# Kernel optimization log

Hardware: AMD Instinct MI355X
Metric: run time of the kernel (lower is better)

The kernel has to match this reference:

```python
import jax, jax.numpy as jnp
import numpy as np

N = 131072
E = 524288
H = 128
EPS = 1e-5

def _layernorm(h, g, b):
    mu = jnp.mean(h, axis=-1, keepdims=True)
    var = jnp.mean((h - mu) ** 2, axis=-1, keepdims=True)
    return (h - mu) * jax.lax.rsqrt(var + EPS) * g + b

def _node_to_node(x, senders, receivers, valid, num_nodes, params):
    # two-way (symmetrized) message passing: gather + scatter_add, then MLP+LN
    W1, b1, W2, b2, W3, b3, g, beta = params
    tws = jnp.concatenate([senders, receivers])
    twr = jnp.concatenate([receivers, senders])
    msg = x[tws]  # [2E', H] gather
    if valid is not None:
        msg = jnp.where(jnp.concatenate([valid, valid])[:, None], msg, 0.0)
    agg = jax.ops.segment_sum(msg, twr, num_segments=num_nodes)  # scatter_add
    h = jax.nn.gelu(agg @ W1 + b1, approximate=False)
    h = jax.nn.gelu(h @ W2 + b2, approximate=False)
    h = h @ W3 + b3
    return _layernorm(h, g, beta)

def setup_inputs() -> dict:
    key = jax.random.key(0)
    ks = jax.random.split(key, 20)
    s = 0.05
    inp = {
        "x": jax.random.normal(ks[0], (N, H), dtype=jnp.float32),
        "edge_index": jax.random.randint(ks[1], (2, E), 0, N, dtype=jnp.int32),
        "pool_p": jax.random.normal(ks[2], (H,), dtype=jnp.float32),
    }
    names = ["dW1", "db1", "dW2", "db2", "dW3", "db3", "dg", "dbeta",
             "uW1", "ub1", "uW2", "ub2", "uW3", "ub3", "ug", "ubeta"]
    shapes = [(H, H), (H,), (H, H), (H,), (H, H), (H,), (H,), (H,),
              (2 * H, H), (H,), (H, H), (H,), (H, H), (H,), (H,), (H,)]
    for i, (nm, sh) in enumerate(zip(names, shapes)):
        if nm in ("dg", "ug"):
            inp[nm] = jnp.ones(sh, dtype=jnp.float32)
        elif nm in ("dbeta", "ubeta") or nm.startswith(("db", "ub")):
            inp[nm] = jnp.zeros(sh, dtype=jnp.float32)
        else:
            inp[nm] = jax.random.normal(ks[3 + i], sh, dtype=jnp.float32) * s
    return inp

def reference(x, edge_index, pool_p,
              dW1, db1, dW2, db2, dW3, db3, dg, dbeta,
              uW1, ub1, uW2, ub2, uW3, ub3, ug, ubeta):
    senders, receivers = edge_index[0], edge_index[1]
    k = N // 2  # TopKPooling ratio=0.5

    # ---- down: TopKPooling ----
    score = x @ pool_p / jnp.linalg.norm(pool_p)  # [N]
    _, perm = jax.lax.top_k(score, k)             # kept node indices
    x_skip = x
    x_p = x[perm] * jnp.tanh(score[perm])[:, None]  # [k, H]
    mask = jnp.zeros((N,), dtype=bool).at[perm].set(True)
    mapping = jnp.zeros((N,), dtype=jnp.int32).at[perm].set(
        jnp.arange(k, dtype=jnp.int32))
    valid = mask[senders] & mask[receivers]
    ps, pr = mapping[senders], mapping[receivers]

    # down conv on pooled graph
    x_d = _node_to_node(x_p, ps, pr, valid, k,
                        (dW1, db1, dW2, db2, dW3, db3, dg, dbeta))

    # ---- up: unpool (indexed scatter write) + skip concat + up conv ----
    recovered = jnp.zeros_like(x_skip).at[perm].set(x_d)
    x_u = jnp.concatenate([recovered, x_skip], axis=-1)  # [N, 2H]
    out = _node_to_node(x_u, senders, receivers, None, N,
                        (uW1, ub1, uW2, ub2, uW3, ub3, ug, ubeta))
    return out
```

## Files before the change

kernel.cpp:

```cpp
#include <hip/hip_runtime.h>

#define N_NODES 131072
#define N_EDGES 524288
#define K_TOP   65536
#define LN_EPS  1e-5f
#define N_TILES (N_NODES / 64)
#define K_TILES (K_TOP / 64)
#define BCAP    5120u

typedef unsigned int u32;
typedef unsigned short u16;
typedef unsigned long long u64;

typedef __attribute__((ext_vector_type(8))) short bf8;
typedef __attribute__((ext_vector_type(4))) float f4;

#define ST_OFF    0
#define CANON_OFF (64u<<10)
#define PART_OFF  (576u<<10)
#define KEYS_OFF  (1u<<20)
#define TVAL_OFF  (2u<<20)
#define KEPT_OFF  ((2u<<20)+(512u<<10))
#define SBUF_OFF  (3u<<20)
#define ADJ_OFF   (35u<<20)


#define C_DW1 0
#define C_DB1 16384
#define C_DW2 16512
#define C_DB2 32896
#define C_DW3 33024
#define C_DB3 49408
#define C_DG  49536
#define C_DBE 49664
#define C_UW1 49792
#define C_UB1 82560
#define C_UW2 82688
#define C_UB2 99072
#define C_UW3 99200
#define C_UB3 115584
#define C_UG  115712
#define C_UBE 115840
#define C_TOT 115968
#define CT_DW1 115968
#define CT_DW2 132352
#define CT_DW3 148736
#define CT_UW1 165120
#define CT_UW2 197888
#define CT_UW3 214272
#define CT_TOT 230656

__device__ __forceinline__ float bflo(u32 u){ return __uint_as_float(u << 16); }
__device__ __forceinline__ float bfhi(u32 u){ return __uint_as_float(u & 0xFFFF0000u); }
__device__ __forceinline__ float bf2f(u16 v){ return __uint_as_float(((u32)v) << 16); }
__device__ __forceinline__ u32 f2bf(float f){
  u32 u = __float_as_uint(f);
  return (u + 0x7FFFu + ((u >> 16) & 1u)) >> 16;
}
__device__ __forceinline__ float gelu_f(float x){
  return 0.5f * x * (1.0f + erff(x * 0.7071067811865476f));
}
__device__ __forceinline__ float2 f2add(float2 a, float2 b){
  return make_float2(a.x + b.x, a.y + b.y);
}

__device__ __forceinline__ int swz16(int row, int cc){
  return row * 128 + ((cc ^ (row & 15)) * 8);
}

__device__ __forceinline__ bf8 ld_bf16_chunk(const u32* __restrict__ rowp, int s, int quad){
  uint4 v = *(const uint4*)(rowp + s * 16 + quad * 4);
  return __builtin_bit_cast(bf8, v);
}
__device__ __forceinline__ bf8 scale_bf16_chunk(const u32* __restrict__ rowp, int s, int quad, float tv){
  uint4 v = *(const uint4*)(rowp + s * 16 + quad * 4);
  uint4 q;
  q.x = f2bf(bflo(v.x) * tv) | (f2bf(bfhi(v.x) * tv) << 16);
  q.y = f2bf(bflo(v.y) * tv) | (f2bf(bfhi(v.y) * tv) << 16);
  q.z = f2bf(bflo(v.z) * tv) | (f2bf(bfhi(v.z) * tv) << 16);
  q.w = f2bf(bflo(v.w) * tv) | (f2bf(bfhi(v.w) * tv) << 16);
  return __builtin_bit_cast(bf8, q);
}
__device__ __forceinline__ bf8 cvt_f32_chunk(const float* __restrict__ rowp, int s, int quad, float tv){
  const float* p = rowp + s * 32 + quad * 8;
  float4 f0 = *(const float4*)p;
  float4 f1 = *(const float4*)(p + 4);
  uint4 q;
  q.x = f2bf(f0.x * tv) | (f2bf(f0.y * tv) << 16);
  q.y = f2bf(f0.z * tv) | (f2bf(f0.w * tv) << 16);
  q.z = f2bf(f1.x * tv) | (f2bf(f1.y * tv) << 16);
  q.w = f2bf(f1.z * tv) | (f2bf(f1.w * tv) << 16);
  return __builtin_bit_cast(bf8, q);
}

__device__ __forceinline__ void gemm_ab(const u16* ws, const bf8 a[4], int mn, int quad, f4 acc[8]){
  #pragma unroll
  for (int s = 0; s < 4; s++){
    #pragma unroll
    for (int j = 0; j < 8; j++){
      bf8 b = *(const bf8*)&ws[swz16(j * 16 + mn, s * 4 + quad)];
      acc[j] = __builtin_amdgcn_mfma_f32_16x16x32_bf16(a[s], b, acc[j], 0, 0, 0);
    }
  }
}

struct SelState {
  u64 prefix;
  u32 krem, eqcnt;
  int is_f32;
  u32 pad;
  double inv_norm;
  u32 eqlist[4096];
  u64 eqkey[4096];
};

struct P16 { const void* q[16]; };

__device__ __forceinline__ void chain_step(const u32* __restrict__ tots, int q,
                                           u32* sfx, u32* selb, int t,
                                           u64& pref, u32& target){
  sfx[t] = tots[q * 256 + t];
  __syncthreads();
  for (int o = 1; o < 256; o <<= 1){
    u32 x = (t + o < 256) ? sfx[t + o] : 0u;
    __syncthreads();
    sfx[t] += x;
    __syncthreads();
  }
  u32 above = (t == 255) ? 0u : sfx[t + 1];
  if (sfx[t] >= target && above < target){ selb[0] = (u32)t; selb[1] = target - above; }
  __syncthreads();
  pref = (pref << 8) | (u64)selb[0];
  target = selb[1];
  __syncthreads();
}

__global__ void k_detect(const u32* __restrict__ xw, SelState* st){
  int t = threadIdx.x;
  int cnt = 0;
  for (int i = t; i < 4096; i += 256){
    u32 w = xw[(size_t)i * 2048];
    u32 e = (w >> 23) & 0xFFu;
    if (e >= 97u && e <= 135u) cnt++;
  }
  __shared__ int sh[256];
  sh[t] = cnt; __syncthreads();
  for (int o = 128; o > 0; o >>= 1){ if (t < o) sh[t] += sh[t+o]; __syncthreads(); }
  if (t == 0){
    st->is_f32 = (sh[0] >= 3072) ? 1 : 0;
    st->prefix = 0; st->krem = K_TOP; st->eqcnt = 0;
  }
}

__global__ void k_canon(P16 ps, const SelState* __restrict__ st, u16* __restrict__ canon,
                        u32* __restrict__ tots, u32* __restrict__ gcur){
  int i = blockIdx.x * 256 + threadIdx.x;
  if (i < 1024) tots[i] = 0u;
  if (i < 256)  gcur[i] = (u32)i * BCAP;
  if (i >= CT_TOT) return;
  int isf = st->is_f32;
  if (i < C_TOT){
    const int off[17] = {C_DW1,C_DB1,C_DW2,C_DB2,C_DW3,C_DB3,C_DG,C_DBE,
                         C_UW1,C_UB1,C_UW2,C_UB2,C_UW3,C_UB3,C_UG,C_UBE,C_TOT};
    int seg = 0;
    #pragma unroll
    for (int s2 = 0; s2 < 16; s2++) if (i >= off[s2+1]) seg = s2 + 1;
    int j = i - off[seg];
    if (isf) canon[i] = (u16)f2bf(((const float*)ps.q[seg])[j]);
    else     canon[i] = ((const u16*)ps.q[seg])[j];
  } else {
    const int dst[7] = {CT_DW1, CT_DW2, CT_DW3, CT_UW1, CT_UW2, CT_UW3, CT_TOT};
    const int wq[6]  = {0, 2, 4, 8, 10, 12};
    int g = i;
    int seg = 0;
    #pragma unroll
    for (int s2 = 0; s2 < 6; s2++) if (g >= dst[s2+1]) seg = s2 + 1;
    int loc = g - dst[seg];
    int K = (seg == 3) ? 256 : 128;
    int n = loc / K, k = loc % K;
    int src = k * 128 + n;
    if (isf) canon[g] = (u16)f2bf(((const float*)ps.q[wq[seg]])[src]);
    else     canon[g] = ((const u16*)ps.q[wq[seg]])[src];
  }
}

__global__ __launch_bounds__(256) void k_score(const void* __restrict__ xraw, const void* __restrict__ praw,
                        const SelState* __restrict__ st,
                        u64* __restrict__ keys, float* __restrict__ tval){
  int t = threadIdx.x, lane = t & 63, w = t >> 6;
  int n = blockIdx.x * 4 + w;
  double d, ps;
  if (st->is_f32){
    const float* xf = (const float*)xraw + (size_t)n * 128;
    const float* pf = (const float*)praw;
    double p0 = (double)pf[lane], p1 = (double)pf[64 + lane];
    d  = (double)xf[lane] * p0 + (double)xf[64 + lane] * p1;
    ps = p0 * p0 + p1 * p1;
  } else {
    const u32* xw = (const u32*)xraw + (size_t)n * 64;
    const u32* pw = (const u32*)praw;
    u32 xx = xw[lane], pv = pw[lane];
    double p0 = (double)bflo(pv), p1 = (double)bfhi(pv);
    d  = (double)bflo(xx) * p0 + (double)bfhi(xx) * p1;
    ps = p0 * p0 + p1 * p1;
  }
  for (int o = 32; o > 0; o >>= 1){
    d  += __shfl_down(d,  o, 64);
    ps += __shfl_down(ps, o, 64);
  }
  if (lane == 0){
    double sc = d * (1.0 / sqrt(ps));
    u64 u = (u64)__double_as_longlong(sc);
    u64 key = (u & 0x8000000000000000ULL) ? ~u : (u | 0x8000000000000000ULL);
    keys[n] = key;
    tval[n] = tanhf((float)sc);
  }
}

__global__ __launch_bounds__(256) void k_histp(const u64* __restrict__ keys,
                                               u32* __restrict__ tots, int pass){
  __shared__ u32 sfx[256];
  __shared__ u32 selb[2];
  __shared__ u32 h[256];
  int t = threadIdx.x;
  u64 pref = 0;
  u32 target = K_TOP;
  for (int q = 0; q < pass; q++)
    chain_step(tots, q, sfx, selb, t, pref, target);
  h[t] = 0;
  __syncthreads();
  int sh_d = 56 - 8 * pass;
  for (int n = blockIdx.x * 256 + t; n < N_NODES; n += 256 * 256){
    u64 k = keys[n];
    bool m = (pass == 0) ? true : ((k >> (sh_d + 8)) == pref);
    if (m) atomicAdd(&h[(u32)((k >> sh_d) & 255)], 1u);
  }
  __syncthreads();
  if (h[t]) atomicAdd(&tots[pass * 256 + t], h[t]);
}

__global__ __launch_bounds__(256) void k_mark(const u64* __restrict__ keys,
                                              const u32* __restrict__ tots,
                                              SelState* st, u32* __restrict__ kept){
  __shared__ u32 sfx[256];
  __shared__ u32 selb[2];
  int t = threadIdx.x;
  u64 pref = 0;
  u32 target = K_TOP;
  for (int q = 0; q < 4; q++)
    chain_step(tots, q, sfx, selb, t, pref, target);
  u32 T = (u32)pref;
  int n = blockIdx.x * 256 + t;
  u64 k = keys[n];
  u32 t32 = (u32)(k >> 32);
  kept[n] = (t32 > T) ? 1u : 0u;
  if (t32 == T){
    u32 i = atomicAdd(&st->eqcnt, 1u);
    if (i < 4096){ st->eqlist[i] = (u32)n; st->eqkey[i] = k; }
  }
}

__global__ __launch_bounds__(256) void k_tie(const u32* __restrict__ tots,
                                             SelState* st, u32* __restrict__ kept){
  __shared__ u32 sfx[256];
  __shared__ u32 selb[2];
  int t = threadIdx.x;
  u64 pref = 0;
  u32 target = K_TOP;
  for (int q = 0; q < 4; q++)
    chain_step(tots, q, sfx, selb, t, pref, target);
  u32 r = target;
  u32 m = st->eqcnt; if (m > 4096) m = 4096;
  for (u32 i = t; i < m; i += 256){
    u64 ki = st->eqkey[i]; u32 ii = st->eqlist[i];
    u32 rank = 0;
    for (u32 j = 0; j < m; j++){
      u64 kj = st->eqkey[j];
      rank += (kj > ki || (kj == ki && st->eqlist[j] < ii)) ? 1u : 0u;
    }
    if (rank < r) kept[ii] = 1u;
  }
}

__global__ __launch_bounds__(256) void k_psum(const u32* __restrict__ kept, u32* __restrict__ bsum){
  __shared__ u32 sh[256];
  int t = threadIdx.x;
  sh[t] = kept[blockIdx.x * 256 + t];
  __syncthreads();
  for (int o = 128; o > 0; o >>= 1){ if (t < o) sh[t] += sh[t+o]; __syncthreads(); }
  if (t == 0) bsum[blockIdx.x] = sh[0];
}

__global__ void k_pscan(u32* __restrict__ bsum){
  __shared__ u32 ex2[256];
  int t = threadIdx.x;
  u32 c0 = bsum[2 * t], c1 = bsum[2 * t + 1];
  ex2[t] = c0 + c1;
  __syncthreads();
  for (int o = 1; o < 256; o <<= 1){
    u32 x = (t >= o) ? ex2[t - o] : 0u;
    __syncthreads();
    ex2[t] += x;
    __syncthreads();
  }
  u32 e0 = ex2[t] - c0 - c1;
  bsum[2 * t] = e0;
  bsum[2 * t + 1] = e0 + c0;
}

__global__ __launch_bounds__(256) void k_pwrite(const u32* __restrict__ kept,
                                                const u32* __restrict__ bsum,
                                                u32* __restrict__ perm){
  __shared__ u32 sc[256];
  int t = threadIdx.x;
  int n = blockIdx.x * 256 + t;
  u32 kp = kept[n];
  sc[t] = kp;
  __syncthreads();
  for (int o = 1; o < 256; o <<= 1){
    u32 x = (t >= o) ? sc[t - o] : 0u;
    __syncthreads();
    sc[t] += x;
    __syncthreads();
  }
  if (kp) perm[bsum[blockIdx.x] + sc[t] - 1u] = (u32)n;
}

__global__ __launch_bounds__(256) void k_bin(const int* __restrict__ se, const int* __restrict__ re,
                                             u32* __restrict__ gcur, u32* __restrict__ pairs){
  __shared__ u32 cnt[256], sc[256], base[256], cur[256], gpos[256];
  __shared__ u32 stage[8192];
  int t = threadIdx.x;
  cnt[t] = 0;
  __syncthreads();
  int e0 = blockIdx.x * 4096;
  for (int i = t; i < 4096; i += 256){
    int s = se[e0 + i], r = re[e0 + i];
    atomicAdd(&cnt[(u32)r >> 9], 1u);
    atomicAdd(&cnt[(u32)s >> 9], 1u);
  }
  __syncthreads();
  sc[t] = cnt[t];
  __syncthreads();
  for (int o = 1; o < 256; o <<= 1){
    u32 x = (t >= o) ? sc[t - o] : 0u;
    __syncthreads();
    sc[t] += x;
    __syncthreads();
  }
  base[t] = sc[t] - cnt[t];
  cur[t] = base[t];
  gpos[t] = atomicAdd(&gcur[t], cnt[t]);
  __syncthreads();
  for (int i = t; i < 4096; i += 256){
    u32 s = (u32)se[e0 + i], r = (u32)re[e0 + i];
    u32 b1 = r >> 9, p1 = ((r & 511u) << 17) | s;
    u32 b2 = s >> 9, p2 = ((s & 511u) << 17) | r;
    stage[atomicAdd(&cur[b1], 1u)] = p1;
    stage[atomicAdd(&cur[b2], 1u)] = p2;
  }
  __syncthreads();
  int lane = t & 63, wv = t >> 6;
  for (int b = wv; b < 256; b += 4){
    u32 n = cnt[b], src = base[b], dst = gpos[b];
    for (u32 i = lane; i < n; i += 64)
      pairs[dst + i] = stage[src + i];
  }
}

__global__ __launch_bounds__(256) void k_place(const u32* __restrict__ gcur,
                                               const u32* __restrict__ pairs,
                                               const u32* __restrict__ kept,
                                               u32* __restrict__ adj,
                                               u32* __restrict__ off, u32* __restrict__ cnts){
  __shared__ u32 cnt[512], ck[512], curk[512], curn[512], lo[512], ex2[256];
  int b = blockIdx.x, t = threadIdx.x;
  u32 base = (u32)b * BCAP;
  u32 total = gcur[b] - base;
  cnt[t] = 0; cnt[t + 256] = 0;
  ck[t] = 0;  ck[t + 256] = 0;
  curk[t] = 0; curk[t + 256] = 0;
  curn[t] = 0; curn[t + 256] = 0;
  __syncthreads();
  for (u32 i = t; i < total; i += 256){
    u32 p = pairs[base + i];
    u32 nl = p >> 17, m = p & 0x1FFFFu;
    atomicAdd(&cnt[nl], 1u);
    if (kept[m]) atomicAdd(&ck[nl], 1u);
  }
  __syncthreads();
  u32 c0 = cnt[2 * t], c1 = cnt[2 * t + 1];
  ex2[t] = c0 + c1;
  __syncthreads();
  for (int o = 1; o < 256; o <<= 1){
    u32 x = (t >= o) ? ex2[t - o] : 0u;
    __syncthreads();
    ex2[t] += x;
    __syncthreads();
  }
  u32 e0 = ex2[t] - c0 - c1;
  int n0 = b * 512 + 2 * t;
  off[n0]     = base + e0;
  off[n0 + 1] = base + e0 + c0;
  cnts[n0]     = (ck[2 * t] << 16) | c0;
  cnts[n0 + 1] = (ck[2 * t + 1] << 16) | c1;
  lo[2 * t] = e0; lo[2 * t + 1] = e0 + c0;
  __syncthreads();
  for (u32 i = t; i < total; i += 256){
    u32 p = pairs[base + i];
    u32 nl = p >> 17, m = p & 0x1FFFFu;
    u32 slot;
    if (kept[m]) slot = base + lo[nl] + atomicAdd(&curk[nl], 1u);
    else         slot = base + lo[nl] + ck[nl] + atomicAdd(&curn[nl], 1u);
    adj[slot] = m;
  }
}


__global__ __launch_bounds__(256, 3) void k_proj_down(
    const void* __restrict__ xraw, const float* __restrict__ tval,
    const u16* __restrict__ W1T, const SelState* __restrict__ st,
    const u32* __restrict__ kept, u32* __restrict__ S)
{
  __shared__ u16 w1s[128 * 128];
  __shared__ u16 os[64 * 128];
  int t = threadIdx.x, lane = t & 63, wv = t >> 6;
  int m0 = wv * 16, mn = lane & 15, quad = lane >> 4;

  for (int i = t; i < 2048; i += 256){
    int row = i >> 4, cc = i & 15;
    *(uint4*)&w1s[swz16(row, cc)] = *(const uint4*)(W1T + row * 128 + cc * 8);
  }
  int isf = st->is_f32;
  __syncthreads();

  for (int tile = blockIdx.x; tile < N_TILES; tile += gridDim.x){
    int row0 = tile * 64;
    int arow = row0 + m0 + mn;
    float tv = tval[arow];
    bf8 a[4];
    if (isf){
      const float* xf = (const float*)xraw + (size_t)arow * 128;
      #pragma unroll
      for (int s = 0; s < 4; s++) a[s] = cvt_f32_chunk(xf, s, quad, tv);
    } else {
      const u32* xw = (const u32*)xraw + (size_t)arow * 64;
      #pragma unroll
      for (int s = 0; s < 4; s++) a[s] = scale_bf16_chunk(xw, s, quad, tv);
    }
    f4 acc[8];
    #pragma unroll
    for (int j = 0; j < 8; j++){ acc[j][0]=0.f; acc[j][1]=0.f; acc[j][2]=0.f; acc[j][3]=0.f; }
    gemm_ab(w1s, a, mn, quad, acc);

    #pragma unroll
    for (int j = 0; j < 8; j++){
      int c = j * 16 + mn;
      #pragma unroll
      for (int rg = 0; rg < 4; rg++){
        int row = m0 + quad * 4 + rg;
        os[row * 128 + ((c >> 3) ^ (row & 15)) * 8 + (c & 7)] = (u16)f2bf(acc[j][rg]);
      }
    }
    __builtin_amdgcn_wave_barrier();
    int rl = m0 + (lane >> 2), qt = lane & 3;
    u32 kp = kept[row0 + rl];
    u32* out = S + (size_t)(row0 + rl) * 64;
    if (kp){
      #pragma unroll
      for (int i = 0; i < 4; i++){
        int cc = qt * 4 + i;
        *(uint4*)(out + cc * 4) = *(const uint4*)&os[swz16(rl, cc)];
      }
    }
    __builtin_amdgcn_wave_barrier();
  }
}

__global__ __launch_bounds__(256, 2) void k_proj_up(
    const u32* __restrict__ R, const void* __restrict__ xraw,
    const u16* __restrict__ W1T, const SelState* __restrict__ st,
    const u32* __restrict__ kept, u32* __restrict__ S2)
{
  __shared__ u16 was[128 * 128];
  __shared__ u16 wbs[128 * 128];
  __shared__ u16 os[64 * 128];
  int t = threadIdx.x, lane = t & 63, wv = t >> 6;
  int m0 = wv * 16, mn = lane & 15, quad = lane >> 4;

  for (int i = t; i < 2048; i += 256){
    int row = i >> 4, cc = i & 15;
    *(uint4*)&was[swz16(row, cc)] = *(const uint4*)(W1T + row * 256 + cc * 8);
    *(uint4*)&wbs[swz16(row, cc)] = *(const uint4*)(W1T + row * 256 + 128 + cc * 8);
  }
  int isf = st->is_f32;
  __syncthreads();

  for (int tile = blockIdx.x; tile < N_TILES; tile += gridDim.x){
    int row0 = tile * 64;
    int arow = row0 + m0 + mn;
    bf8 a[4];
    u32 kp = kept[arow];
    const u32* rp = R + (size_t)arow * 64;
    #pragma unroll
    for (int s = 0; s < 4; s++){
      if (kp) a[s] = ld_bf16_chunk(rp, s, quad);
      else { uint4 z = {0,0,0,0}; a[s] = __builtin_bit_cast(bf8, z); }
    }
    f4 acc[8];
    #pragma unroll
    for (int j = 0; j < 8; j++){ acc[j][0]=0.f; acc[j][1]=0.f; acc[j][2]=0.f; acc[j][3]=0.f; }
    gemm_ab(was, a, mn, quad, acc);

    if (isf){
      const float* xf = (const float*)xraw + (size_t)arow * 128;
      #pragma unroll
      for (int s = 0; s < 4; s++) a[s] = cvt_f32_chunk(xf, s, quad, 1.0f);
    } else {
      const u32* xw = (const u32*)xraw + (size_t)arow * 64;
      #pragma unroll
      for (int s = 0; s < 4; s++) a[s] = ld_bf16_chunk(xw, s, quad);
    }
    gemm_ab(wbs, a, mn, quad, acc);

    #pragma unroll
    for (int j = 0; j < 8; j++){
      int c = j * 16 + mn;
      #pragma unroll
      for (int rg = 0; rg < 4; rg++){
        int row = m0 + quad * 4 + rg;
        os[row * 128 + ((c >> 3) ^ (row & 15)) * 8 + (c & 7)] = (u16)f2bf(acc[j][rg]);
      }
    }
    __builtin_amdgcn_wave_barrier();
    int rl = m0 + (lane >> 2), qt = lane & 3;
    u32* out = S2 + (size_t)(row0 + rl) * 64;
    #pragma unroll
    for (int i = 0; i < 4; i++){
      int cc = qt * 4 + i;
      *(uint4*)(out + cc * 4) = *(const uint4*)&os[swz16(rl, cc)];
    }
    __builtin_amdgcn_wave_barrier();
  }
}

__device__ __forceinline__ void agg_row(const u32* __restrict__ Smsg, const u32* __restrict__ adj,
                                        u32 jb, u32 je, int lane, float b1l, float b1h,
                                        u32* __restrict__ Hrow){
  float2 a = make_float2(0.f, 0.f);
  u32 j = jb;
  for (; j + 8 <= je; j += 8){
    u32 e0 = adj[j],   e1 = adj[j+1], e2 = adj[j+2], e3 = adj[j+3];
    u32 e4 = adj[j+4], e5 = adj[j+5], e6 = adj[j+6], e7 = adj[j+7];
    u32 w0 = Smsg[(size_t)e0 * 64 + lane];
    u32 w1 = Smsg[(size_t)e1 * 64 + lane];
    u32 w2 = Smsg[(size_t)e2 * 64 + lane];
    u32 w3 = Smsg[(size_t)e3 * 64 + lane];
    u32 w4 = Smsg[(size_t)e4 * 64 + lane];
    u32 w5 = Smsg[(size_t)e5 * 64 + lane];
    u32 w6 = Smsg[(size_t)e6 * 64 + lane];
    u32 w7 = Smsg[(size_t)e7 * 64 + lane];
    float2 v0 = make_float2(bflo(w0), bfhi(w0));
    float2 v1 = make_float2(bflo(w1), bfhi(w1));
    float2 v2 = make_float2(bflo(w2), bfhi(w2));
    float2 v3 = make_float2(bflo(w3), bfhi(w3));
    float2 v4 = make_float2(bflo(w4), bfhi(w4));
    float2 v5 = make_float2(bflo(w5), bfhi(w5));
    float2 v6 = make_float2(bflo(w6), bfhi(w6));
    float2 v7 = make_float2(bflo(w7), bfhi(w7));
    a = f2add(a, f2add(f2add(f2add(v0, v1), f2add(v2, v3)),
                       f2add(f2add(v4, v5), f2add(v6, v7))));
  }
  for (; j + 4 <= je; j += 4){
    u32 e0 = adj[j], e1 = adj[j+1], e2 = adj[j+2], e3 = adj[j+3];
    u32 w0 = Smsg[(size_t)e0 * 64 + lane];
    u32 w1 = Smsg[(size_t)e1 * 64 + lane];
    u32 w2 = Smsg[(size_t)e2 * 64 + lane];
    u32 w3 = Smsg[(size_t)e3 * 64 + lane];
    float2 v0 = make_float2(bflo(w0), bfhi(w0));
    float2 v1 = make_float2(bflo(w1), bfhi(w1));
    float2 v2 = make_float2(bflo(w2), bfhi(w2));
    float2 v3 = make_float2(bflo(w3), bfhi(w3));
    a = f2add(a, f2add(f2add(v0, v1), f2add(v2, v3)));
  }
  for (; j < je; j++){
    u32 w = Smsg[(size_t)adj[j] * 64 + lane];
    a = f2add(a, make_float2(bflo(w), bfhi(w)));
  }
  Hrow[lane] = f2bf(gelu_f(a.x + b1l)) | (f2bf(gelu_f(a.y + b1h)) << 16);
}

__global__ __launch_bounds__(256, 4) void k_agg_up(
    const u32* __restrict__ Smsg, const u32* __restrict__ off, const u32* __restrict__ cnts,
    const u32* __restrict__ adj, const u16* __restrict__ cb1,
    u32* __restrict__ H)
{
  int t = threadIdx.x, lane = t & 63, wv = t >> 6;
  float b1l = bf2f(cb1[2 * lane]), b1h = bf2f(cb1[2 * lane + 1]);
  int base = blockIdx.x * 16 + wv * 4;
  #pragma unroll 1
  for (int rr = 0; rr < 4; rr++){
    int n = base + rr;
    u32 jb = off[n];
    agg_row(Smsg, adj, jb, jb + (cnts[n] & 0xFFFFu), lane, b1l, b1h, H + (size_t)n * 64);
  }
}

__global__ __launch_bounds__(256, 4) void k_agg_down(
    const u32* __restrict__ Smsg, const u32* __restrict__ off, const u32* __restrict__ cnts,
    const u32* __restrict__ adj, const u16* __restrict__ cb1,
    const u32* __restrict__ perm, u32* __restrict__ H)
{
  int t = threadIdx.x, lane = t & 63, wv = t >> 6;
  float b1l = bf2f(cb1[2 * lane]), b1h = bf2f(cb1[2 * lane + 1]);
  int base = blockIdx.x * 16 + wv * 4;
  #pragma unroll 1
  for (int rr = 0; rr < 4; rr++){
    int n = (int)perm[base + rr];
    u32 jb = off[n];
    agg_row(Smsg, adj, jb, jb + (cnts[n] >> 16), lane, b1l, b1h, H + (size_t)n * 64);
  }
}

template<int IS_DOWN>
__global__ __launch_bounds__(256, 2) void k_mlp(
    const u32* __restrict__ H,
    const u16* __restrict__ cW2T, const u16* __restrict__ cb2,
    const u16* __restrict__ cW3T, const u16* __restrict__ cb3,
    const u16* __restrict__ cg, const u16* __restrict__ cbe,
    const u32* __restrict__ perm, const SelState* __restrict__ st,
    u32* __restrict__ Rout, void* __restrict__ fout)
{
  __shared__ u16 w2s[128 * 128];
  __shared__ u16 w3s[128 * 128];
  __shared__ u16 os[64 * 128];
  int t = threadIdx.x, lane = t & 63, wv = t >> 6;
  int m0 = wv * 16, mn = lane & 15, quad = lane >> 4;

  for (int i = t; i < 2048; i += 256){
    int row = i >> 4, cc = i & 15;
    *(uint4*)&w2s[swz16(row, cc)] = *(const uint4*)(cW2T + row * 128 + cc * 8);
    *(uint4*)&w3s[swz16(row, cc)] = *(const uint4*)(cW3T + row * 128 + cc * 8);
  }
  float b2v[8], b3v[8], gv[8], bev[8];
  #pragma unroll
  for (int j = 0; j < 8; j++){
    int c = j * 16 + mn;
    b2v[j] = bf2f(cb2[c]); b3v[j] = bf2f(cb3[c]);
    gv[j]  = bf2f(cg[c]);  bev[j] = bf2f(cbe[c]);
  }
  int isf = st->is_f32;
  int ntiles = IS_DOWN ? K_TILES : N_TILES;
  __syncthreads();

  for (int tile = blockIdx.x; tile < ntiles; tile += gridDim.x){
    int row0 = tile * 64;
    int arow = IS_DOWN ? (int)perm[row0 + m0 + mn] : (row0 + m0 + mn);

    bf8 a[4];
    const u32* hp = H + (size_t)arow * 64;
    #pragma unroll
    for (int s = 0; s < 4; s++) a[s] = ld_bf16_chunk(hp, s, quad);
    f4 acc[8];
    #pragma unroll
    for (int j = 0; j < 8; j++){ acc[j][0]=0.f; acc[j][1]=0.f; acc[j][2]=0.f; acc[j][3]=0.f; }
    gemm_ab(w2s, a, mn, quad, acc);

    #pragma unroll
    for (int j = 0; j < 8; j++){
      int c = j * 16 + mn;
      #pragma unroll
      for (int rg = 0; rg < 4; rg++){
        int row = m0 + quad * 4 + rg;
        os[row * 128 + ((c >> 3) ^ (row & 15)) * 8 + (c & 7)] = (u16)f2bf(gelu_f(acc[j][rg] + b2v[j]));
      }
    }
    __builtin_amdgcn_wave_barrier();

    #pragma unroll
    for (int s = 0; s < 4; s++) a[s] = *(const bf8*)&os[swz16(m0 + mn, s * 4 + quad)];
    #pragma unroll
    for (int j = 0; j < 8; j++){ acc[j][0]=0.f; acc[j][1]=0.f; acc[j][2]=0.f; acc[j][3]=0.f; }
    gemm_ab(w3s, a, mn, quad, acc);

    #pragma unroll
    for (int j = 0; j < 8; j++){
      #pragma unroll
      for (int rg = 0; rg < 4; rg++) acc[j][rg] += b3v[j];
    }
    float s1[4] = {0.f,0.f,0.f,0.f}, s2[4] = {0.f,0.f,0.f,0.f};
    #pragma unroll
    for (int j = 0; j < 8; j++){
      #pragma unroll
      for (int rg = 0; rg < 4; rg++){
        float v = acc[j][rg];
        s1[rg] += v; s2[rg] += v * v;
      }
    }
    #pragma unroll
    for (int o = 1; o < 16; o <<= 1){
      #pragma unroll
      for (int rg = 0; rg < 4; rg++){
        s1[rg] += __shfl_xor(s1[rg], o, 64);
        s2[rg] += __shfl_xor(s2[rg], o, 64);
      }
    }
    float mu[4], rs[4];
    #pragma unroll
    for (int rg = 0; rg < 4; rg++){
      mu[rg] = s1[rg] * 0.0078125f;
      float var = s2[rg] * 0.0078125f - mu[rg] * mu[rg];
      rs[rg] = rsqrtf(var + LN_EPS);
    }
    #pragma unroll
    for (int j = 0; j < 8; j++){
      #pragma unroll
      for (int rg = 0; rg < 4; rg++)
        acc[j][rg] = (acc[j][rg] - mu[rg]) * rs[rg] * gv[j] + bev[j];
    }

    if (!IS_DOWN && isf){
      float* fo = (float*)fout;
      #pragma unroll
      for (int j = 0; j < 8; j++){
        #pragma unroll
        for (int rg = 0; rg < 4; rg++)
          fo[(size_t)(row0 + m0 + quad * 4 + rg) * 128 + j * 16 + mn] = acc[j][rg];
      }
      continue;
    }

    __builtin_amdgcn_wave_barrier();
    #pragma unroll
    for (int j = 0; j < 8; j++){
      int c = j * 16 + mn;
      #pragma unroll
      for (int rg = 0; rg < 4; rg++){
        int row = m0 + quad * 4 + rg;
        os[row * 128 + ((c >> 3) ^ (row & 15)) * 8 + (c & 7)] = (u16)f2bf(acc[j][rg]);
      }
    }
    __builtin_amdgcn_wave_barrier();
    int rl = m0 + (lane >> 2), qt = lane & 3;
    int orow = IS_DOWN ? (int)perm[row0 + rl] : (row0 + rl);
    u32* out = (IS_DOWN ? Rout : (u32*)fout) + (size_t)orow * 64;
    #pragma unroll
    for (int i = 0; i < 4; i++){
      int cc = qt * 4 + i;
      *(uint4*)(out + cc * 4) = *(const uint4*)&os[swz16(rl, cc)];
    }
    __builtin_amdgcn_wave_barrier();
  }
}


extern "C" void kernel_launch(void* const* d_in, const int* in_sizes, int n_in,
                              void* d_out, int out_size, void* d_ws, size_t ws_size,
                              hipStream_t stream)
{
  const void* x     = d_in[0];
  const int* eidx   = (const int*)d_in[1];
  const void* poolp = d_in[2];
  const int* senders = eidx;
  const int* receivers = eidx + N_EDGES;

  char* ws = (char*)d_ws;
  SelState* st = (SelState*)(ws + ST_OFF);
  u16*  canon  = (u16*) (ws + CANON_OFF);
  u32*  tots   = (u32*) (ws + PART_OFF);
  u32*  gcur   = (u32*) (ws + PART_OFF + 4096);
  u32*  bsum   = (u32*) (ws + PART_OFF + 8192);
  u32*  perm   = (u32*) (ws + PART_OFF + 16384);
  u64*  keys   = (u64*) (ws + KEYS_OFF);
  u32*  off    = (u32*) (ws + KEYS_OFF);
  u32*  cnts   = (u32*) (ws + KEYS_OFF + (512u<<10));
  float* tval  = (float*)(ws + TVAL_OFF);
  u32*  kept   = (u32*) (ws + KEPT_OFF);
  u32*  Sbuf   = (u32*) (ws + SBUF_OFF);
  u32*  adj    = (u32*) (ws + ADJ_OFF);
  u32*  pairs  = Sbuf;
  u32*  Dbuf   = (u32*) d_out;

  P16 ps;
  for (int i = 0; i < 16; i++) ps.q[i] = d_in[3 + i];

  k_detect<<<1, 256, 0, stream>>>((const u32*)x, st);
  k_canon<<<(CT_TOT + 255) / 256, 256, 0, stream>>>(ps, st, canon, tots, gcur);
  k_score<<<N_NODES / 4, 256, 0, stream>>>(x, poolp, st, keys, tval);
  for (int pass = 0; pass < 4; pass++)
    k_histp<<<256, 256, 0, stream>>>(keys, tots, pass);
  k_mark<<<N_NODES / 256, 256, 0, stream>>>(keys, tots, st, kept);
  k_tie<<<1, 256, 0, stream>>>(tots, st, kept);

  k_psum<<<N_NODES / 256, 256, 0, stream>>>(kept, bsum);
  k_pscan<<<1, 256, 0, stream>>>(bsum);
  k_pwrite<<<N_NODES / 256, 256, 0, stream>>>(kept, bsum, perm);

  k_bin<<<N_EDGES / 4096, 256, 0, stream>>>(senders, receivers, gcur, pairs);
  k_place<<<256, 256, 0, stream>>>(gcur, pairs, kept, adj, off, cnts);

  k_proj_down<<<768, 256, 0, stream>>>(x, tval, canon + CT_DW1, st, kept, Sbuf);
  k_agg_down<<<K_TOP / 16, 256, 0, stream>>>(Sbuf, off, cnts, adj, canon + C_DB1, perm, Dbuf);
  k_mlp<1><<<512, 256, 0, stream>>>(Dbuf,
      canon + CT_DW2, canon + C_DB2, canon + CT_DW3, canon + C_DB3,
      canon + C_DG, canon + C_DBE, perm, st, Sbuf, nullptr);

  k_proj_up<<<512, 256, 0, stream>>>(Sbuf, x, canon + CT_UW1, st, kept, Dbuf);
  k_agg_up<<<N_NODES / 16, 256, 0, stream>>>(Dbuf, off, cnts, adj, canon + C_UB1, Sbuf);
  k_mlp<0><<<512, 256, 0, stream>>>(Sbuf,
      canon + CT_UW2, canon + C_UB2, canon + CT_UW3, canon + C_UB3,
      canon + C_UG, canon + C_UBE, perm, st, nullptr, d_out);
}
```

Measured before the change: 442.0 us.

## Store pooled features compactly by rank and prefetch next MLP tile

k_pwrite now writes each kept node's rank+1 into the kept array. The down-path aggregation and MLP store pooled rows in compact rank order rather than node-indexed order, so k_mlp no longer needs perm lookups, and k_proj_up reads rows through the rank. k_mlp also loads the next tile's input rows before computing the current tile, overlapping global latency with the GEMMs. This costs extra registers for the prefetched fragments and changes the meaning of kept, which every other consumer must treat only as nonzero.

After: 455.0 us. +2.9%, slower.

```diff
diff --git a/kernel.cpp b/kernel.cpp
--- a/kernel.cpp
+++ b/kernel.cpp
@@ -308,7 +308,7 @@
   bsum[2 * t + 1] = e0 + c0;
 }
 
-__global__ __launch_bounds__(256) void k_pwrite(const u32* __restrict__ kept,
+__global__ __launch_bounds__(256) void k_pwrite(u32* __restrict__ kept,
                                                 const u32* __restrict__ bsum,
                                                 u32* __restrict__ perm){
   __shared__ u32 sc[256];
@@ -323,7 +323,11 @@
     sc[t] += x;
     __syncthreads();
   }
-  if (kp) perm[bsum[blockIdx.x] + sc[t] - 1u] = (u32)n;
+  if (kp){
+    u32 pos = bsum[blockIdx.x] + sc[t] - 1u;
+    perm[pos] = (u32)n;
+    kept[n] = pos + 1u;
+  }
 }
 
 __global__ __launch_bounds__(256) void k_bin(const int* __restrict__ se, const int* __restrict__ re,
@@ -501,7 +505,7 @@
     int arow = row0 + m0 + mn;
     bf8 a[4];
     u32 kp = kept[arow];
-    const u32* rp = R + (size_t)arow * 64;
+    const u32* rp = R + (size_t)(kp - 1u) * 64;
     #pragma unroll
     for (int s = 0; s < 4; s++){
       if (kp) a[s] = ld_bf16_chunk(rp, s, quad);
@@ -616,9 +620,10 @@
   int base = blockIdx.x * 16 + wv * 4;
   #pragma unroll 1
   for (int rr = 0; rr < 4; rr++){
-    int n = (int)perm[base + rr];
+    int idx = base + rr;
+    int n = (int)perm[idx];
     u32 jb = off[n];
-    agg_row(Smsg, adj, jb, jb + (cnts[n] >> 16), lane, b1l, b1h, H + (size_t)n * 64);
+    agg_row(Smsg, adj, jb, jb + (cnts[n] >> 16), lane, b1l, b1h, H + (size_t)idx * 64);
   }
 }
 
@@ -628,7 +633,7 @@
     const u16* __restrict__ cW2T, const u16* __restrict__ cb2,
     const u16* __restrict__ cW3T, const u16* __restrict__ cb3,
     const u16* __restrict__ cg, const u16* __restrict__ cbe,
-    const u32* __restrict__ perm, const SelState* __restrict__ st,
+    const SelState* __restrict__ st,
     u32* __restrict__ Rout, void* __restrict__ fout)
 {
   __shared__ u16 w2s[128 * 128];
@@ -650,17 +655,27 @@
     gv[j]  = bf2f(cg[c]);  bev[j] = bf2f(cbe[c]);
   }
   int isf = st->is_f32;
-  int ntiles = IS_DOWN ? K_TILES : N_TILES;
-  __syncthreads();
+  const int ntiles = IS_DOWN ? K_TILES : N_TILES;
+  __syncthreads();
+
+  bf8 a[4];
+  {
+    const u32* hp = H + (size_t)(blockIdx.x * 64 + m0 + mn) * 64;
+    #pragma unroll
+    for (int s = 0; s < 4; s++) a[s] = ld_bf16_chunk(hp, s, quad);
+  }
 
   for (int tile = blockIdx.x; tile < ntiles; tile += gridDim.x){
     int row0 = tile * 64;
-    int arow = IS_DOWN ? (int)perm[row0 + m0 + mn] : (row0 + m0 + mn);
-
-    bf8 a[4];
-    const u32* hp = H + (size_t)arow * 64;
-    #pragma unroll
-    for (int s = 0; s < 4; s++) a[s] = ld_bf16_chunk(hp, s, quad);
+    int ntile = tile + gridDim.x;
+    bool hasn = ntile < ntiles;
+    bf8 an[4];
+    if (hasn){
+      const u32* hp = H + (size_t)(ntile * 64 + m0 + mn) * 64;
+      #pragma unroll
+      for (int s = 0; s < 4; s++) an[s] = ld_bf16_chunk(hp, s, quad);
+    }
+
     f4 acc[8];
     #pragma unroll
     for (int j = 0; j < 8; j++){ acc[j][0]=0.f; acc[j][1]=0.f; acc[j][2]=0.f; acc[j][3]=0.f; }
@@ -677,11 +692,12 @@
     }
     __builtin_amdgcn_wave_barrier();
 
-    #pragma unroll
-    for (int s = 0; s < 4; s++) a[s] = *(const bf8*)&os[swz16(m0 + mn, s * 4 + quad)];
+    bf8 a2[4];
+    #pragma unroll
+    for (int s = 0; s < 4; s++) a2[s] = *(const bf8*)&os[swz16(m0 + mn, s * 4 + quad)];
     #pragma unroll
     for (int j = 0; j < 8; j++){ acc[j][0]=0.f; acc[j][1]=0.f; acc[j][2]=0.f; acc[j][3]=0.f; }
-    gemm_ab(w3s, a, mn, quad, acc);
+    gemm_ab(w3s, a2, mn, quad, acc);
 
     #pragma unroll
     for (int j = 0; j < 8; j++){
@@ -727,6 +743,8 @@
         for (int rg = 0; rg < 4; rg++)
           fo[(size_t)(row0 + m0 + quad * 4 + rg) * 128 + j * 16 + mn] = acc[j][rg];
       }
+      #pragma unroll
+      for (int s = 0; s < 4; s++) a[s] = an[s];
       continue;
     }
 
@@ -742,14 +760,15 @@
     }
     __builtin_amdgcn_wave_barrier();
     int rl = m0 + (lane >> 2), qt = lane & 3;
-    int orow = IS_DOWN ? (int)perm[row0 + rl] : (row0 + rl);
-    u32* out = (IS_DOWN ? Rout : (u32*)fout) + (size_t)orow * 64;
+    u32* out = (IS_DOWN ? Rout : (u32*)fout) + (size_t)(row0 + rl) * 64;
     #pragma unroll
     for (int i = 0; i < 4; i++){
       int cc = qt * 4 + i;
       *(uint4*)(out + cc * 4) = *(const uint4*)&os[swz16(rl, cc)];
     }
     __builtin_amdgcn_wave_barrier();
+    #pragma unroll
+    for (int s = 0; s < 4; s++) a[s] = an[s];
   }
 }
 
@@ -803,11 +822,11 @@
   k_agg_down<<<K_TOP / 16, 256, 0, stream>>>(Sbuf, off, cnts, adj, canon + C_DB1, perm, Dbuf);
   k_mlp<1><<<512, 256, 0, stream>>>(Dbuf,
       canon + CT_DW2, canon + C_DB2, canon + CT_DW3, canon + C_DB3,
-      canon + C_DG, canon + C_DBE, perm, st, Sbuf, nullptr);
+      canon + C_DG, canon + C_DBE, st, Sbuf, nullptr);
 
   k_proj_up<<<512, 256, 0, stream>>>(Sbuf, x, canon + CT_UW1, st, kept, Dbuf);
   k_agg_up<<<N_NODES / 16, 256, 0, stream>>>(Dbuf, off, cnts, adj, canon + C_UB1, Sbuf);
   k_mlp<0><<<512, 256, 0, stream>>>(Sbuf,
       canon + CT_UW2, canon + C_UB2, canon + CT_UW3, canon + C_UB3,
-      canon + C_UG, canon + C_UBE, perm, st, nullptr, d_out);
-}
+      canon + C_UG, canon + C_UBE, st, nullptr, d_out);
+}
```
